# Kernel optimization log

Measured on AMD Instinct MI355X. Metric: run time of the kernel, lower is better.

Reference implementation:

```python
import jax, jax.numpy as jnp
import numpy as np

D_MODEL = 1024
N_HEADS = 16
HEAD_DIM = D_MODEL // N_HEADS


def setup_inputs() -> dict:
    key = jax.random.key(0)
    ks = jax.random.split(key, 5)
    B, T = 2, 2048
    x = jax.random.normal(ks[0], (B, T, D_MODEL), dtype=jnp.float32)
    s = 1.0 / np.sqrt(D_MODEL)
    qkv_w = jax.random.uniform(ks[1], (3 * D_MODEL, D_MODEL), jnp.float32, -s, s)
    qkv_b = jax.random.uniform(ks[2], (3 * D_MODEL,), jnp.float32, -s, s)
    out_w = jax.random.uniform(ks[3], (D_MODEL, D_MODEL), jnp.float32, -s, s)
    out_b = jax.random.uniform(ks[4], (D_MODEL,), jnp.float32, -s, s)
    return {"x": x, "qkv_w": qkv_w, "qkv_b": qkv_b, "out_w": out_w, "out_b": out_b}


def reference(x, qkv_w, qkv_b, out_w, out_b):
    B, T, _ = x.shape
    # qkv projection: [B,T,3*D]
    qkv = x @ qkv_w.T + qkv_b
    qkv = qkv.reshape(B, T, 3, N_HEADS, HEAD_DIM)
    qkv = jnp.transpose(qkv, (2, 0, 3, 1, 4))  # [3,B,H,T,Hd]
    q, k, v = qkv[0], qkv[1], qkv[2]
    scale = 1.0 / np.sqrt(HEAD_DIM)
    scores = jnp.einsum("bhqd,bhkd->bhqk", q, k) * scale  # [B,H,T,T]
    causal = jnp.tril(jnp.ones((T, T), dtype=bool))
    scores = jnp.where(causal, scores, -jnp.inf)
    weights = jax.nn.softmax(scores, axis=-1)
    # dropout in eval mode (identity)
    out = jnp.einsum("bhqk,bhkd->bhqd", weights, v)  # [B,H,T,Hd]
    out = jnp.transpose(out, (0, 2, 1, 3)).reshape(B, T, D_MODEL)
    return out @ out_w.T + out_b
```

## Files before the change

### kernel.cpp

```cpp
#include <hip/hip_runtime.h>
#include <hip/hip_bf16.h>


typedef __bf16 bf16;
typedef bf16 bf16x8 __attribute__((ext_vector_type(8)));
typedef bf16 bf16x4 __attribute__((ext_vector_type(4)));
typedef float f32x4 __attribute__((ext_vector_type(4)));

#define MFMA16(a, b, c) __builtin_amdgcn_mfma_f32_16x16x32_bf16((a), (b), (c), 0, 0, 0)

static constexpr int D_MODEL = 1024;
static constexpr int NH = 16;
static constexpr int HD = 64;
static constexpr int SEQ = 2048;
static constexpr int NB = 2;
static constexpr float QSCALE = 0.125f * 1.44269504088896340736f;

__device__ __forceinline__ bf16x8 cvt8(const float* p) {
    float4 u0 = *(const float4*)p;
    float4 u1 = *(const float4*)(p + 4);
    bf16x8 v = { (bf16)u0.x, (bf16)u0.y, (bf16)u0.z, (bf16)u0.w,
                 (bf16)u1.x, (bf16)u1.y, (bf16)u1.z, (bf16)u1.w };
    return v;
}

__device__ __forceinline__ void async16(const bf16* g, bf16* l) {
    __builtin_amdgcn_global_load_lds(
        (const __attribute__((address_space(1))) void*)g,
        (__attribute__((address_space(3))) void*)l, 16, 0, 0);
}

__global__ __launch_bounds__(256)
void k_cast(const float* __restrict__ in, bf16* __restrict__ out, int n8)
{
    int i = blockIdx.x * 256 + threadIdx.x;
    if (i < n8) *(bf16x8*)&out[(size_t)i * 8] = cvt8(&in[(size_t)i * 8]);
}

__global__ __launch_bounds__(256)
void k_qkv(const bf16* __restrict__ x, const bf16* __restrict__ w,
           const float* __restrict__ bias,
           bf16* __restrict__ Qb, bf16* __restrict__ Kb, bf16* __restrict__ VbT)
{
    __shared__ bf16 As[128 * 32];
    __shared__ bf16 Ws[128 * 32];

    const int tid  = threadIdx.x;
    const int wv   = tid >> 6;
    const int lane = tid & 63;
    const int lr   = lane & 15;
    const int lk   = lane >> 4;
    const int wm   = wv >> 1, wn = wv & 1;
    const int m0   = blockIdx.x * 128;
    const int n0   = blockIdx.y * 128;

    const int sRow = tid >> 2;
    const int sCol = (tid & 3) * 8;
    const int sOff = sRow * 32 + sCol;

    f32x4 acc[4][4] = {};

    for (int kt = 0; kt < 1024; kt += 32) {
        __syncthreads();
        async16(&x[(size_t)(m0 + sRow     ) * 1024 + kt + sCol], &As[sOff]);
        async16(&x[(size_t)(m0 + 64 + sRow) * 1024 + kt + sCol], &As[64 * 32 + sOff]);
        async16(&w[(size_t)(n0 + sRow     ) * 1024 + kt + sCol], &Ws[sOff]);
        async16(&w[(size_t)(n0 + 64 + sRow) * 1024 + kt + sCol], &Ws[64 * 32 + sOff]);
        __syncthreads();

        bf16x8 a[4], b[4];
        #pragma unroll
        for (int i = 0; i < 4; i++) {
            a[i] = *(const bf16x8*)&As[(wm * 64 + i * 16 + lr) * 32 + lk * 8];
            b[i] = *(const bf16x8*)&Ws[(wn * 64 + i * 16 + lr) * 32 + lk * 8];
        }
        #pragma unroll
        for (int i = 0; i < 4; i++)
            #pragma unroll
            for (int j = 0; j < 4; j++)
                acc[i][j] = MFMA16(a[i], b[j], acc[i][j]);
    }

    #pragma unroll
    for (int i = 0; i < 4; i++) {
        #pragma unroll
        for (int j = 0; j < 4; j++) {
            const int gm0 = m0 + wm * 64 + i * 16 + lk * 4;
            const int gn  = n0 + wn * 64 + j * 16 + lr;
            const int sel = gn >> 10;
            const int rem = gn & 1023;
            const int h   = rem >> 6;
            const int hd  = rem & 63;
            const int bb  = gm0 >> 11;
            const int t0  = gm0 & 2047;
            if (sel == 2) {
                bf16x4 p;
                #pragma unroll
                for (int r = 0; r < 4; r++) p[r] = (bf16)(acc[i][j][r] + bias[gn]);
                *(bf16x4*)&VbT[((size_t)(bb * NH + h) * HD + hd) * SEQ + t0] = p;
            } else {
                #pragma unroll
                for (int r = 0; r < 4; r++) {
                    float v = acc[i][j][r] + bias[gn];
                    size_t idx = ((size_t)(bb * NH + h) * SEQ + t0 + r) * HD + hd;
                    if (sel == 0) Qb[idx] = (bf16)(v * QSCALE);
                    else          Kb[idx] = (bf16)v;
                }
            }
        }
    }
}

__global__ __launch_bounds__(256)
void k_attn(const bf16* __restrict__ Qb, const bf16* __restrict__ Kb,
            const bf16* __restrict__ VbT, bf16* __restrict__ AO)
{
    __shared__ bf16 Ks[64][72];
    __shared__ bf16 Vt[64][72];
    __shared__ bf16 Ps[64][72];

    const int tid  = threadIdx.x;
    const int wv   = tid >> 6;
    const int lane = tid & 63;
    const int lr   = lane & 15;
    const int lk   = lane >> 4;
    const int bh   = blockIdx.y;
    const int qt   = ((bh >> 3) & 1) ? (31 - (int)blockIdx.x) : (int)blockIdx.x;

    const bf16* Qp  = Qb  + (size_t)bh * SEQ * HD;
    const bf16* Kp  = Kb  + (size_t)bh * SEQ * HD;
    const bf16* Vtp = VbT + (size_t)bh * HD * SEQ;

    const int qg = qt * 64 + wv * 16 + lr;

    bf16x8 qf[2];
    qf[0] = *(const bf16x8*)&Qp[(size_t)qg * HD +      lk * 8];
    qf[1] = *(const bf16x8*)&Qp[(size_t)qg * HD + 32 + lk * 8];

    f32x4 ot[4] = {};
    float lsum = 0.f;

    const int r0 = tid >> 3;
    const int c0 = (tid & 7) * 8;

    for (int kt = 0; kt <= qt; kt++) {
        const int k0 = kt * 64;
        __syncthreads();
        *(bf16x8*)&Ks[r0     ][c0] = *(const bf16x8*)&Kp[(size_t)(k0 + r0     ) * HD + c0];
        *(bf16x8*)&Ks[r0 + 32][c0] = *(const bf16x8*)&Kp[(size_t)(k0 + r0 + 32) * HD + c0];
        *(bf16x8*)&Vt[r0     ][c0] = *(const bf16x8*)&Vtp[(size_t)(r0     ) * SEQ + k0 + c0];
        *(bf16x8*)&Vt[r0 + 32][c0] = *(const bf16x8*)&Vtp[(size_t)(r0 + 32) * SEQ + k0 + c0];
        __syncthreads();

        f32x4 s[4] = {};
        #pragma unroll
        for (int j = 0; j < 4; j++) {
            #pragma unroll
            for (int c = 0; c < 2; c++) {
                bf16x8 ka = *(const bf16x8*)&Ks[j * 16 + lr][c * 32 + lk * 8];
                s[j] = MFMA16(ka, qf[c], s[j]);
            }
        }

        const bool diag = (kt == qt);
        #pragma unroll
        for (int j = 0; j < 4; j++) {
            const int keyb = k0 + j * 16 + lk * 4;
            f32x4 p;
            #pragma unroll
            for (int r = 0; r < 4; r++) {
                float e = __builtin_amdgcn_exp2f(s[j][r]);
                if (diag) e = (keyb + r > qg) ? 0.f : e;
                p[r] = e;
            }
            s[j] = p;
            lsum += (p[0] + p[1]) + (p[2] + p[3]);
        }

        #pragma unroll
        for (int j = 0; j < 4; j++) {
            bf16x4 p4 = { (bf16)s[j][0], (bf16)s[j][1], (bf16)s[j][2], (bf16)s[j][3] };
            *(bf16x4*)&Ps[wv * 16 + lr][j * 16 + lk * 4] = p4;
        }

        #pragma unroll
        for (int c = 0; c < 2; c++) {
            bf16x8 pb = *(const bf16x8*)&Ps[wv * 16 + lr][c * 32 + lk * 8];
            #pragma unroll
            for (int jh = 0; jh < 4; jh++) {
                bf16x8 va = *(const bf16x8*)&Vt[jh * 16 + lr][c * 32 + lk * 8];
                ot[jh] = MFMA16(va, pb, ot[jh]);
            }
        }
    }

    lsum += __shfl_xor(lsum, 16);
    lsum += __shfl_xor(lsum, 32);

    const float inv = 1.0f / lsum;
    const int b_ = bh >> 4, h_ = bh & 15;
    const size_t base = ((size_t)(b_ * SEQ + qg)) * D_MODEL + h_ * HD;
    #pragma unroll
    for (int jh = 0; jh < 4; jh++) {
        bf16x4 o4 = { (bf16)(ot[jh][0] * inv), (bf16)(ot[jh][1] * inv),
                      (bf16)(ot[jh][2] * inv), (bf16)(ot[jh][3] * inv) };
        *(bf16x4*)&AO[base + jh * 16 + lk * 4] = o4;
    }
}

__global__ __launch_bounds__(256)
void k_oproj(const bf16* __restrict__ a_, const bf16* __restrict__ w,
             const float* __restrict__ bias, float* __restrict__ out)
{
    __shared__ bf16 As[128 * 32];
    __shared__ bf16 Ws[64 * 32];

    const int tid  = threadIdx.x;
    const int wv   = tid >> 6;
    const int lane = tid & 63;
    const int lr   = lane & 15;
    const int lk   = lane >> 4;
    const int wm   = wv >> 1, wn = wv & 1;
    const int m0   = blockIdx.x * 128;
    const int n0   = blockIdx.y * 64;

    const int sRow = tid >> 2;
    const int sCol = (tid & 3) * 8;
    const int sOff = sRow * 32 + sCol;

    f32x4 acc[4][2] = {};

    for (int kt = 0; kt < 1024; kt += 32) {
        __syncthreads();
        async16(&a_[(size_t)(m0 + sRow     ) * 1024 + kt + sCol], &As[sOff]);
        async16(&a_[(size_t)(m0 + 64 + sRow) * 1024 + kt + sCol], &As[64 * 32 + sOff]);
        async16(&w [(size_t)(n0 + sRow     ) * 1024 + kt + sCol], &Ws[sOff]);
        __syncthreads();

        bf16x8 a[4], b[2];
        #pragma unroll
        for (int i = 0; i < 4; i++)
            a[i] = *(const bf16x8*)&As[(wm * 64 + i * 16 + lr) * 32 + lk * 8];
        #pragma unroll
        for (int j = 0; j < 2; j++)
            b[j] = *(const bf16x8*)&Ws[(wn * 32 + j * 16 + lr) * 32 + lk * 8];
        #pragma unroll
        for (int i = 0; i < 4; i++)
            #pragma unroll
            for (int j = 0; j < 2; j++)
                acc[i][j] = MFMA16(a[i], b[j], acc[i][j]);
    }

    #pragma unroll
    for (int i = 0; i < 4; i++) {
        #pragma unroll
        for (int j = 0; j < 2; j++) {
            #pragma unroll
            for (int r = 0; r < 4; r++) {
                int gm = m0 + wm * 64 + i * 16 + lk * 4 + r;
                int gn = n0 + wn * 32 + j * 16 + lr;
                out[(size_t)gm * 1024 + gn] = acc[i][j][r] + bias[gn];
            }
        }
    }
}

extern "C" void kernel_launch(void* const* d_in, const int* in_sizes, int n_in,
                              void* d_out, int out_size, void* d_ws, size_t ws_size,
                              hipStream_t stream)
{
    const float* x     = (const float*)d_in[0];
    const float* qkv_w = (const float*)d_in[1];
    const float* qkv_b = (const float*)d_in[2];
    const float* out_w = (const float*)d_in[3];
    const float* out_b = (const float*)d_in[4];
    float* out = (float*)d_out;

    const size_t SZ = (size_t)NB * NH * SEQ * HD;
    bf16* Qb  = (bf16*)d_ws;
    bf16* Kb  = Qb + SZ;
    bf16* VbT = Kb + SZ;
    bf16* AO  = VbT + SZ;
    bf16* xb  = AO + SZ;
    bf16* wqb = xb + SZ;
    bf16* wob = wqb + (size_t)3 * D_MODEL * D_MODEL;

    hipLaunchKernelGGL(k_cast, dim3(2048), dim3(256), 0, stream, x,     xb,  524288);
    hipLaunchKernelGGL(k_cast, dim3(1536), dim3(256), 0, stream, qkv_w, wqb, 393216);
    hipLaunchKernelGGL(k_cast, dim3(512),  dim3(256), 0, stream, out_w, wob, 131072);

    hipLaunchKernelGGL(k_qkv, dim3(32, 24), dim3(256), 0, stream,
                       xb, wqb, qkv_b, Qb, Kb, VbT);
    hipLaunchKernelGGL(k_attn, dim3(32, 32), dim3(256), 0, stream,
                       Qb, Kb, VbT, AO);
    hipLaunchKernelGGL(k_oproj, dim3(32, 16), dim3(256), 0, stream,
                       AO, wob, out_b, out);
}
```

Measured before the change: 203.1 us.

## Process 128 queries per attention block to reuse K/V tiles across two halves

The attention kernel now gives each workgroup 128 query rows (two 64-row halves per wave) instead of 64, so each K/V tile loaded into shared memory feeds twice as many MFMAs. The grid shrinks from 1024 to 512 blocks with a 1-D index that interleaves heads and pairs light and heavy causal tiles. The aim is to halve global-to-LDS K/V traffic and barrier overhead per unit of work. In exchange it uses more registers, a larger LDS P buffer, more masked work on the diagonal tiles, and fewer blocks to spread across CUs.

```diff
diff --git a/kernel.cpp b/kernel.cpp
--- a/kernel.cpp
+++ b/kernel.cpp
@@ -117,33 +117,41 @@
 {
     __shared__ bf16 Ks[64][72];
     __shared__ bf16 Vt[64][72];
-    __shared__ bf16 Ps[64][72];
+    __shared__ bf16 Ps[128][72];
 
     const int tid  = threadIdx.x;
     const int wv   = tid >> 6;
     const int lane = tid & 63;
     const int lr   = lane & 15;
     const int lk   = lane >> 4;
-    const int bh   = blockIdx.y;
-    const int qt   = ((bh >> 3) & 1) ? (31 - (int)blockIdx.x) : (int)blockIdx.x;
+
+    const int id = blockIdx.x;
+    const int bh = id & 31;
+    const int u  = id >> 5;
+    const int qt = (u < 8) ? u : (23 - u);
 
     const bf16* Qp  = Qb  + (size_t)bh * SEQ * HD;
     const bf16* Kp  = Kb  + (size_t)bh * SEQ * HD;
     const bf16* Vtp = VbT + (size_t)bh * HD * SEQ;
 
-    const int qg = qt * 64 + wv * 16 + lr;
-
-    bf16x8 qf[2];
-    qf[0] = *(const bf16x8*)&Qp[(size_t)qg * HD +      lk * 8];
-    qf[1] = *(const bf16x8*)&Qp[(size_t)qg * HD + 32 + lk * 8];
-
-    f32x4 ot[4] = {};
-    float lsum = 0.f;
+    const int qbase = qt * 128;
+    const int qg[2] = { qbase + wv * 16 + lr, qbase + 64 + wv * 16 + lr };
+
+    bf16x8 qf[2][2];
+    #pragma unroll
+    for (int h = 0; h < 2; h++)
+        #pragma unroll
+        for (int c = 0; c < 2; c++)
+            qf[h][c] = *(const bf16x8*)&Qp[(size_t)qg[h] * HD + c * 32 + lk * 8];
+
+    f32x4 ot[2][4] = {};
+    float lsum[2] = { 0.f, 0.f };
 
     const int r0 = tid >> 3;
     const int c0 = (tid & 7) * 8;
 
-    for (int kt = 0; kt <= qt; kt++) {
+    const int nkt = 2 * qt + 2;
+    for (int kt = 0; kt < nkt; kt++) {
         const int k0 = kt * 64;
         __syncthreads();
         *(bf16x8*)&Ks[r0     ][c0] = *(const bf16x8*)&Kp[(size_t)(k0 + r0     ) * HD + c0];
@@ -152,59 +160,74 @@
         *(bf16x8*)&Vt[r0 + 32][c0] = *(const bf16x8*)&Vtp[(size_t)(r0 + 32) * SEQ + k0 + c0];
         __syncthreads();
 
-        f32x4 s[4] = {};
+        f32x4 s[2][4] = {};
         #pragma unroll
         for (int j = 0; j < 4; j++) {
             #pragma unroll
             for (int c = 0; c < 2; c++) {
                 bf16x8 ka = *(const bf16x8*)&Ks[j * 16 + lr][c * 32 + lk * 8];
-                s[j] = MFMA16(ka, qf[c], s[j]);
-            }
-        }
-
-        const bool diag = (kt == qt);
-        #pragma unroll
-        for (int j = 0; j < 4; j++) {
-            const int keyb = k0 + j * 16 + lk * 4;
-            f32x4 p;
-            #pragma unroll
-            for (int r = 0; r < 4; r++) {
-                float e = __builtin_amdgcn_exp2f(s[j][r]);
-                if (diag) e = (keyb + r > qg) ? 0.f : e;
-                p[r] = e;
-            }
-            s[j] = p;
-            lsum += (p[0] + p[1]) + (p[2] + p[3]);
-        }
-
-        #pragma unroll
-        for (int j = 0; j < 4; j++) {
-            bf16x4 p4 = { (bf16)s[j][0], (bf16)s[j][1], (bf16)s[j][2], (bf16)s[j][3] };
-            *(bf16x4*)&Ps[wv * 16 + lr][j * 16 + lk * 4] = p4;
-        }
+                s[0][j] = MFMA16(ka, qf[0][c], s[0][j]);
+                s[1][j] = MFMA16(ka, qf[1][c], s[1][j]);
+            }
+        }
+
+        const bool bnd = (kt >= 2 * qt);
+        #pragma unroll
+        for (int h = 0; h < 2; h++) {
+            #pragma unroll
+            for (int j = 0; j < 4; j++) {
+                const int keyb = k0 + j * 16 + lk * 4;
+                f32x4 p;
+                #pragma unroll
+                for (int r = 0; r < 4; r++) {
+                    float e = __builtin_amdgcn_exp2f(s[h][j][r]);
+                    if (bnd) e = (keyb + r > qg[h]) ? 0.f : e;
+                    p[r] = e;
+                }
+                s[h][j] = p;
+                lsum[h] += (p[0] + p[1]) + (p[2] + p[3]);
+            }
+        }
+
+        #pragma unroll
+        for (int h = 0; h < 2; h++)
+            #pragma unroll
+            for (int j = 0; j < 4; j++) {
+                bf16x4 p4 = { (bf16)s[h][j][0], (bf16)s[h][j][1],
+                              (bf16)s[h][j][2], (bf16)s[h][j][3] };
+                *(bf16x4*)&Ps[h * 64 + wv * 16 + lr][j * 16 + lk * 4] = p4;
+            }
 
         #pragma unroll
         for (int c = 0; c < 2; c++) {
-            bf16x8 pb = *(const bf16x8*)&Ps[wv * 16 + lr][c * 32 + lk * 8];
+            bf16x8 pb0 = *(const bf16x8*)&Ps[     wv * 16 + lr][c * 32 + lk * 8];
+            bf16x8 pb1 = *(const bf16x8*)&Ps[64 + wv * 16 + lr][c * 32 + lk * 8];
             #pragma unroll
             for (int jh = 0; jh < 4; jh++) {
                 bf16x8 va = *(const bf16x8*)&Vt[jh * 16 + lr][c * 32 + lk * 8];
-                ot[jh] = MFMA16(va, pb, ot[jh]);
-            }
-        }
-    }
-
-    lsum += __shfl_xor(lsum, 16);
-    lsum += __shfl_xor(lsum, 32);
-
-    const float inv = 1.0f / lsum;
+                ot[0][jh] = MFMA16(va, pb0, ot[0][jh]);
+                ot[1][jh] = MFMA16(va, pb1, ot[1][jh]);
+            }
+        }
+    }
+
+    #pragma unroll
+    for (int h = 0; h < 2; h++) {
+        lsum[h] += __shfl_xor(lsum[h], 16);
+        lsum[h] += __shfl_xor(lsum[h], 32);
+    }
+
     const int b_ = bh >> 4, h_ = bh & 15;
-    const size_t base = ((size_t)(b_ * SEQ + qg)) * D_MODEL + h_ * HD;
-    #pragma unroll
-    for (int jh = 0; jh < 4; jh++) {
-        bf16x4 o4 = { (bf16)(ot[jh][0] * inv), (bf16)(ot[jh][1] * inv),
-                      (bf16)(ot[jh][2] * inv), (bf16)(ot[jh][3] * inv) };
-        *(bf16x4*)&AO[base + jh * 16 + lk * 4] = o4;
+    #pragma unroll
+    for (int h = 0; h < 2; h++) {
+        const float inv = 1.0f / lsum[h];
+        const size_t base = ((size_t)(b_ * SEQ + qg[h])) * D_MODEL + h_ * HD;
+        #pragma unroll
+        for (int jh = 0; jh < 4; jh++) {
+            bf16x4 o4 = { (bf16)(ot[h][jh][0] * inv), (bf16)(ot[h][jh][1] * inv),
+                          (bf16)(ot[h][jh][2] * inv), (bf16)(ot[h][jh][3] * inv) };
+            *(bf16x4*)&AO[base + jh * 16 + lk * 4] = o4;
+        }
     }
 }
 
@@ -291,7 +314,7 @@
 
     hipLaunchKernelGGL(k_qkv, dim3(32, 24), dim3(256), 0, stream,
                        xb, wqb, qkv_b, Qb, Kb, VbT);
-    hipLaunchKernelGGL(k_attn, dim3(32, 32), dim3(256), 0, stream,
+    hipLaunchKernelGGL(k_attn, dim3(512), dim3(256), 0, stream,
                        Qb, Kb, VbT, AO);
     hipLaunchKernelGGL(k_oproj, dim3(32, 16), dim3(256), 0, stream,
                        AO, wob, out_b, out);
```

Result: slower. 218.6 us (+7.6%).
